# Kernel tuning notes

Measured on AMD Instinct MI355X. Metric: run time of the kernel, lower is better.

Reference implementation:

```python
import jax, jax.numpy as jnp
import numpy as np

H = 16            # num heads
D = 64            # head dim
HID = 1024        # hidden size
ALPHA = 1.0       # < 2 -> power-law kernel
BANDWIDTH = 1.0
A = 0.5           # doubly-stochastic exponent
RADIUS = 1.0      # sphere radius
EPS = 1e-7


def setup_inputs() -> dict:
    key = jax.random.key(0)
    ks = jax.random.split(key, 5)
    x = jax.random.normal(ks[0], (2, 2048, HID), dtype=jnp.float32)
    s = 1.0 / np.sqrt(HID)
    qkv_w = jax.random.normal(ks[1], (3 * HID, HID), dtype=jnp.float32) * s
    qkv_b = jnp.zeros((3 * HID,), dtype=jnp.float32)
    out_w = jax.random.normal(ks[2], (HID, HID), dtype=jnp.float32) * s
    out_b = jnp.zeros((HID,), dtype=jnp.float32)
    return {"x": x, "qkv_w": qkv_w, "qkv_b": qkv_b, "out_w": out_w, "out_b": out_b}


def _l2norm(t):
    # torch F.normalize(p=2, dim=-1): divide by max(||t||, 1e-12)
    n = jnp.sqrt(jnp.sum(t * t, axis=-1, keepdims=True))
    return t / jnp.maximum(n, 1e-12)


def reference(x, qkv_w, qkv_b, out_w, out_b):
    B, S, _ = x.shape
    qkv = x @ qkv_w.T + qkv_b                       # [B,S,3*HID]
    q, k, v = jnp.split(qkv, 3, axis=-1)
    # [B,H,S,D]
    q = _l2norm(q.reshape(B, S, H, D).transpose(0, 2, 1, 3))
    k = _l2norm(k.reshape(B, S, H, D).transpose(0, 2, 1, 3))
    v = v.reshape(B, S, H, D).transpose(0, 2, 1, 3)
    # geodesic distance on the sphere
    cos = jnp.clip(jnp.einsum('bhsd,bhtd->bhst', q, k), -1.0 + EPS, 1.0 - EPS)
    g_dist = jnp.arccos(cos) * RADIUS               # [B,H,S,S]
    # alpha < 2: power-law kernel
    attn_score = (1.0 + g_dist / jnp.sqrt(BANDWIDTH)) ** (-(D + ALPHA))
    # doubly-stochastic-style rescale: diag(row^-a) @ K @ diag(col^-a)
    row = attn_score.sum(-1) ** (-A)                # [B,H,S]
    col = attn_score.sum(-2) ** (-A)                # [B,H,S]
    k_tilde = row[..., :, None] * attn_score * col[..., None, :]
    # F.normalize(p=1, dim=3): divide by max(sum |.|, 1e-12); entries >= 0
    probs = k_tilde / jnp.maximum(k_tilde.sum(-1, keepdims=True), 1e-12)
    out = jnp.einsum('bhst,bhtd->bhsd', probs, v)   # [B,H,S,D]
    out = out.transpose(0, 2, 1, 3).reshape(B, S, HID)
    return out @ out_w.T + out_b
```

## Files before the change

kernel.cpp:

```cpp
#include <hip/hip_runtime.h>
#include <math.h>

#define NH   16
#define HD   64
#define HIDN 1024
#define NB   2
#define SEQ  2048
#define ROWS (NB*SEQ)
#define BH   (NB*NH)

typedef __attribute__((ext_vector_type(8))) short bf16x8;
typedef __attribute__((ext_vector_type(8))) _Float16 f16x8;
typedef __attribute__((ext_vector_type(4))) float f32x4;
typedef __attribute__((ext_vector_type(2))) float f32x2;
typedef _Float16 f16;

typedef const __attribute__((address_space(1))) void GV;
typedef __attribute__((address_space(3))) void LV;
__device__ __forceinline__ void glds16(const void* g, void* l) {
    __builtin_amdgcn_global_load_lds((GV*)g, (LV*)l, 16, 0, 0);
}

__device__ __forceinline__ unsigned short f2bf(float f) {
    unsigned u = __float_as_uint(f);
    u += 0x7FFF + ((u >> 16) & 1);
    return (unsigned short)(u >> 16);
}
__device__ __forceinline__ bf16x8 ldfrag(const unsigned short* p) {
    return *(const bf16x8*)p;
}
__device__ __forceinline__ f16x8 ldfragh(const f16* p) {
    return *(const f16x8*)p;
}
__device__ __forceinline__ f32x4 mfma16(bf16x8 a, bf16x8 b, f32x4 c) {
    return __builtin_amdgcn_mfma_f32_16x16x32_bf16(a, b, c, 0, 0, 0);
}
__device__ __forceinline__ f32x4 mfma16h(f16x8 a, f16x8 b, f32x4 c) {
    return __builtin_amdgcn_mfma_f32_16x16x32_f16(a, b, c, 0, 0, 0);
}

__device__ __forceinline__ f32x2 log2_1pacos_pair(float c0, float c1) {
    f32x2 u = { fmaxf(1.0f - c0, 0.0f), fmaxf(1.0f - c1, 0.0f) };
    f32x2 s = { __builtin_amdgcn_sqrtf(u.x), __builtin_amdgcn_sqrtf(u.y) };
    f32x2 p = u * 2.68532e-3f + 7.89259e-3f;
    p = u * p + 2.6516504e-2f;
    p = u * p + 1.1785113e-1f;
    p = u * p + 1.4142136f;
    f32x2 t = s * p + 1.0f;
    return (f32x2){ __builtin_amdgcn_logf(t.x), __builtin_amdgcn_logf(t.y) };
}
__device__ __forceinline__ unsigned packbf(f32x2 w) {
    return (__float_as_uint(w.x) >> 16) | (__float_as_uint(w.y) & 0xffff0000u);
}

__global__ __launch_bounds__(256)
void conv_f16(const float* __restrict__ src, f16* __restrict__ dst) {
    int i = (blockIdx.x * 256 + threadIdx.x) * 8;
    float4 a = *(const float4*)(src + i);
    float4 b = *(const float4*)(src + i + 4);
    f16x8 o = { (f16)a.x, (f16)a.y, (f16)a.z, (f16)a.w,
                (f16)b.x, (f16)b.y, (f16)b.z, (f16)b.w };
    *(f16x8*)(dst + i) = o;
}

__global__ __launch_bounds__(256)
void gemm_nt_f16(const f16* __restrict__ A, const f16* __restrict__ B,
                 const float* __restrict__ bias, float* __restrict__ C,
                 int M, int N, int K)
{
    __shared__ f16 As[128 * 32];
    __shared__ f16 Bs[128 * 32];
    const int tid = threadIdx.x;
    const int lane = tid & 63, w = tid >> 6;
    const int ln = lane & 15, lq = lane >> 4;
    const int wm = (w >> 1) * 64, wn = (w & 1) * 64;
    const int m0 = blockIdx.x * 128, n0 = blockIdx.y * 128;

    const int grow = lane >> 2;
    const int gcol = (lane & 3) * 8;
    const f16* Ab = A + (size_t)(m0 + w * 32 + grow) * K + gcol;
    const f16* Bb = B + (size_t)(n0 + w * 32 + grow) * K + gcol;
    f16* Asw = As + (w * 32) * 32;
    f16* Bsw = Bs + (w * 32) * 32;

    f32x4 acc[4][4];
    #pragma unroll
    for (int i = 0; i < 4; ++i)
        #pragma unroll
        for (int j = 0; j < 4; ++j) acc[i][j] = (f32x4){0.f, 0.f, 0.f, 0.f};

    for (int kc = 0; kc < K; kc += 32) {
        __syncthreads();
        #pragma unroll
        for (int i = 0; i < 2; ++i) {
            glds16(Ab + (size_t)(i * 16) * K + kc, Asw + (i * 16) * 32);
            glds16(Bb + (size_t)(i * 16) * K + kc, Bsw + (i * 16) * 32);
        }
        __syncthreads();
        f16x8 af[4], bf[4];
        #pragma unroll
        for (int i = 0; i < 4; ++i)
            af[i] = *(const f16x8*)&As[(wm + i * 16 + ln) * 32 + lq * 8];
        #pragma unroll
        for (int j = 0; j < 4; ++j)
            bf[j] = *(const f16x8*)&Bs[(wn + j * 16 + ln) * 32 + lq * 8];
        #pragma unroll
        for (int i = 0; i < 4; ++i)
            #pragma unroll
            for (int j = 0; j < 4; ++j)
                acc[i][j] = mfma16h(af[i], bf[j], acc[i][j]);
    }

    #pragma unroll
    for (int i = 0; i < 4; ++i) {
        #pragma unroll
        for (int j = 0; j < 4; ++j) {
            int colIdx = n0 + wn + j * 16 + ln;
            float bs = bias[colIdx];
            #pragma unroll
            for (int r = 0; r < 4; ++r) {
                int row = m0 + wm + i * 16 + lq * 4 + r;
                C[(size_t)row * N + colIdx] = acc[i][j][r] + bs;
            }
        }
    }
}

__global__ __launch_bounds__(256)
void normalize_qk_f16(const float* __restrict__ qkv,
                      f16* __restrict__ qf, f16* __restrict__ kf)
{
    int w    = blockIdx.x * 4 + (threadIdx.x >> 6);
    int lane = threadIdx.x & 63;
    int n = w >> 4, h = w & 15;
    int b = n >> 11, s = n & 2047;
    const float* base = qkv + (size_t)n * 3 * HIDN + h * HD;
    float q = base[lane], k = base[HIDN + lane];
    float qs = q * q, ks = k * k;
    #pragma unroll
    for (int o = 32; o; o >>= 1) { qs += __shfl_xor(qs, o); ks += __shfl_xor(ks, o); }
    q *= 1.0f / fmaxf(sqrtf(qs), 1e-12f);
    k *= 1.0f / fmaxf(sqrtf(ks), 1e-12f);
    size_t idx = ((size_t)((b * NH + h) * SEQ + s)) * HD + lane;
    qf[idx] = (f16)q;
    kf[idx] = (f16)k;
}

__global__ __launch_bounds__(256)
void v_transpose(const float* __restrict__ qkv, unsigned short* __restrict__ vth)
{
    __shared__ float Ls[64][65];
    int bh = blockIdx.y, s0 = blockIdx.x * 64;
    int b = bh >> 4, h = bh & 15;
    int tid = threadIdx.x;
    #pragma unroll
    for (int i = 0; i < 4; ++i) {
        int idx = tid + i * 256;
        int row = idx >> 4, c4 = (idx & 15) * 4;
        float4 v = *(const float4*)&qkv[((size_t)(b * SEQ + s0 + row)) * 3 * HIDN
                                        + 2 * HIDN + h * HD + c4];
        Ls[row][c4+0] = v.x; Ls[row][c4+1] = v.y; Ls[row][c4+2] = v.z; Ls[row][c4+3] = v.w;
    }
    __syncthreads();
    int d = tid >> 2, sb = (tid & 3) * 16;
    unsigned short hi[16];
    #pragma unroll
    for (int j = 0; j < 16; ++j) hi[j] = f2bf(Ls[sb + j][d]);
    size_t o = ((size_t)bh * HD + d) * SEQ + s0 + sb;
    *(uint4*)&vth[o]     = *(uint4*)&hi[0];
    *(uint4*)&vth[o + 8] = *(uint4*)&hi[8];
}

#define KSTR 72

__global__ __launch_bounds__(256)
void col_sum_f16(const f16* __restrict__ qf, const f16* __restrict__ kf,
                 float* __restrict__ colp)
{
    __shared__ __align__(16) f16 Qs[64 * KSTR];
    int bh = blockIdx.y;
    int tid = threadIdx.x, w = tid >> 6, lane = tid & 63, ln = lane & 15, lq = lane >> 4;
    int m0 = blockIdx.x * 64 + w * 16;
    const f16* qb = qf + (size_t)bh * SEQ * HD;
    const int sr = tid >> 3;
    const int sc = (tid & 7) * 8;

    size_t rowK = ((size_t)bh * SEQ + m0 + ln) * HD;
    f16x8 kf0 = ldfragh(kf + rowK + lq * 8), kf1 = ldfragh(kf + rowK + 32 + lq * 8);

    uint4 qa = *(const uint4*)(qb + (size_t)sr * HD + sc);
    uint4 qc = *(const uint4*)(qb + (size_t)(sr + 32) * HD + sc);

    f32x2 cacc01 = {0.f, 0.f}, cacc23 = {0.f, 0.f};
    #pragma unroll 1
    for (int st = 0; st < SEQ / 64; ++st) {
        __syncthreads();
        *(uint4*)&Qs[sr * KSTR + sc] = qa;
        *(uint4*)&Qs[(sr + 32) * KSTR + sc] = qc;
        int sn = (st + 1 < SEQ / 64) ? (st + 1) * 64 : 0;
        qa = *(const uint4*)(qb + (size_t)(sn + sr) * HD + sc);
        qc = *(const uint4*)(qb + (size_t)(sn + sr + 32) * HD + sc);
        __syncthreads();
        #pragma unroll
        for (int nt = 0; nt < 4; ++nt) {
            const f16* qp = &Qs[(nt * 16 + ln) * KSTR + lq * 8];
            f32x4 sacc = {0.f, 0.f, 0.f, 0.f};
            sacc = mfma16h(kf0, *(const f16x8*)qp, sacc);
            sacc = mfma16h(kf1, *(const f16x8*)(qp + 32), sacc);
            f32x2 l01 = log2_1pacos_pair(sacc[0], sacc[1]) * -65.0f;
            f32x2 l23 = log2_1pacos_pair(sacc[2], sacc[3]) * -65.0f;
            cacc01 += (f32x2){ __builtin_amdgcn_exp2f(l01.x),
                               __builtin_amdgcn_exp2f(l01.y) };
            cacc23 += (f32x2){ __builtin_amdgcn_exp2f(l23.x),
                               __builtin_amdgcn_exp2f(l23.y) };
        }
    }
    float cacc[4] = {cacc01.x, cacc01.y, cacc23.x, cacc23.y};
    #pragma unroll
    for (int r = 0; r < 4; ++r) {
        float v = cacc[r];
        v += __shfl_xor(v, 1); v += __shfl_xor(v, 2);
        v += __shfl_xor(v, 4); v += __shfl_xor(v, 8);
        if (ln == 0)
            colp[(size_t)bh * SEQ + m0 + lq * 4 + r] = v;
    }
}

__global__ __launch_bounds__(256)
void col_finalize(const float* __restrict__ colp, float* __restrict__ col)
{
    int i = (blockIdx.x * 256 + threadIdx.x) * 4;
    float4 a = *(const float4*)&colp[i];
    float4 o;
    o.x = -0.5f * __builtin_amdgcn_logf(a.x);
    o.y = -0.5f * __builtin_amdgcn_logf(a.y);
    o.z = -0.5f * __builtin_amdgcn_logf(a.z);
    o.w = -0.5f * __builtin_amdgcn_logf(a.w);
    *(float4*)&col[i] = o;
}

__global__ __launch_bounds__(256)
void attn_f16(const f16* __restrict__ qf, const f16* __restrict__ kf,
              const unsigned short* __restrict__ vth,
              const float* __restrict__ col, f16* __restrict__ ctx)
{
    __shared__ __align__(16) f16 Ks[64 * KSTR];
    __shared__ __align__(16) unsigned short Vs[64 * KSTR];
    __shared__ __align__(16) unsigned short Ws[4][16 * KSTR];
    __shared__ __align__(16) float lcls[64];
    int bh = blockIdx.y;
    int b = bh >> 4, h = bh & 15;
    int tid = threadIdx.x, w = tid >> 6, lane = tid & 63, ln = lane & 15, lq = lane >> 4;
    int m0 = blockIdx.x * 64 + w * 16;
    unsigned short* ws = Ws[w];

    const f16* kb = kf + (size_t)bh * SEQ * HD;
    const unsigned short* vb = vth + (size_t)bh * HD * SEQ;
    const float* cb = col + (size_t)bh * SEQ;

    const int sr = tid >> 3;
    const int sc = (tid & 7) * 8;

    size_t rowQ = ((size_t)bh * SEQ + m0 + ln) * HD;
    f16x8 qf0 = ldfragh(qf + rowQ + lq * 8), qf1 = ldfragh(qf + rowQ + 32 + lq * 8);

    bf16x8 ones;
    #pragma unroll
    for (int i = 0; i < 8; ++i) ones[i] = (short)0x3F80;

    f32x4 num[4];
    #pragma unroll
    for (int nt = 0; nt < 4; ++nt) num[nt] = (f32x4){0.f, 0.f, 0.f, 0.f};
    f32x4 den = {0.f, 0.f, 0.f, 0.f};

    uint4 ka = *(const uint4*)(kb + (size_t)sr * HD + sc);
    uint4 kc = *(const uint4*)(kb + (size_t)(sr + 32) * HD + sc);
    uint4 va = *(const uint4*)(vb + (size_t)sr * SEQ + sc);
    uint4 vc = *(const uint4*)(vb + (size_t)(sr + 32) * SEQ + sc);
    float clv = (tid < 64) ? cb[tid] : 0.f;

    #pragma unroll 1
    for (int tt = 0; tt < SEQ / 64; ++tt) {
        __syncthreads();
        *(uint4*)&Ks[sr * KSTR + sc] = ka;
        *(uint4*)&Ks[(sr + 32) * KSTR + sc] = kc;
        *(uint4*)&Vs[sr * KSTR + sc] = va;
        *(uint4*)&Vs[(sr + 32) * KSTR + sc] = vc;
        if (tid < 64) lcls[tid] = clv;
        int tn = (tt + 1 < SEQ / 64) ? (tt + 1) * 64 : 0;
        ka = *(const uint4*)(kb + (size_t)(tn + sr) * HD + sc);
        kc = *(const uint4*)(kb + (size_t)(tn + sr + 32) * HD + sc);
        va = *(const uint4*)(vb + (size_t)sr * SEQ + tn + sc);
        vc = *(const uint4*)(vb + (size_t)(sr + 32) * SEQ + tn + sc);
        clv = (tid < 64) ? cb[tn + tid] : 0.f;
        __syncthreads();

        #pragma unroll
        for (int nt = 0; nt < 4; ++nt) {
            const f16* kp = &Ks[(nt * 16 + ln) * KSTR + lq * 8];
            f32x4 sacc = {0.f, 0.f, 0.f, 0.f};
            sacc = mfma16h(*(const f16x8*)kp, qf0, sacc);
            sacc = mfma16h(*(const f16x8*)(kp + 32), qf1, sacc);
            float4 cl = *(const float4*)&lcls[nt * 16 + lq * 4];
            f32x2 a01 = log2_1pacos_pair(sacc[0], sacc[1]) * -65.0f
                        + (f32x2){cl.x, cl.y};
            f32x2 a23 = log2_1pacos_pair(sacc[2], sacc[3]) * -65.0f
                        + (f32x2){cl.z, cl.w};
            f32x2 w01 = { __builtin_amdgcn_exp2f(a01.x),
                          __builtin_amdgcn_exp2f(a01.y) };
            f32x2 w23 = { __builtin_amdgcn_exp2f(a23.x),
                          __builtin_amdgcn_exp2f(a23.y) };
            uint2 pw;
            pw.x = packbf(w01);
            pw.y = packbf(w23);
            *(uint2*)(ws + ln * KSTR + nt * 16 + lq * 4) = pw;
        }
        bf16x8 wa0 = ldfrag(ws + ln * KSTR + lq * 8);
        bf16x8 wa1 = ldfrag(ws + ln * KSTR + 32 + lq * 8);
        den = mfma16(wa0, ones, den);
        den = mfma16(wa1, ones, den);
        #pragma unroll
        for (int nt = 0; nt < 4; ++nt) {
            const unsigned short* vp = &Vs[(nt * 16 + ln) * KSTR + lq * 8];
            num[nt] = mfma16(wa0, *(const bf16x8*)vp, num[nt]);
            num[nt] = mfma16(wa1, *(const bf16x8*)(vp + 32), num[nt]);
        }
    }

    #pragma unroll
    for (int r = 0; r < 4; ++r) {
        float inv = 1.0f / fmaxf(den[r], 1e-12f);
        int s = m0 + lq * 4 + r;
        #pragma unroll
        for (int nt = 0; nt < 4; ++nt)
            ctx[((size_t)(b * SEQ + s)) * HIDN + h * HD + nt * 16 + ln] =
                (f16)(num[nt][r] * inv);
    }
}

extern "C" void kernel_launch(void* const* d_in, const int* in_sizes, int n_in,
                              void* d_out, int out_size, void* d_ws, size_t ws_size,
                              hipStream_t stream) {
    const float* x      = (const float*)d_in[0];
    const float* qkv_w  = (const float*)d_in[1];
    const float* qkv_b  = (const float*)d_in[2];
    const float* out_w  = (const float*)d_in[3];
    const float* out_b  = (const float*)d_in[4];
    float* out = (float*)d_out;

    const size_t NTT = (size_t)BH * SEQ * HD;
    float* qkv = (float*)d_ws;
    float* colp = qkv;
    float* col = qkv + (size_t)ROWS * 3 * HIDN;
    f16* xh    = (f16*)(col + (size_t)BH * SEQ);
    f16* wqh   = xh + (size_t)ROWS * HIDN;
    f16* woh   = wqh + (size_t)3 * HIDN * HIDN;
    f16* ctxh  = woh + (size_t)HIDN * HIDN;
    f16* qfp   = ctxh + (size_t)ROWS * HIDN;
    f16* kfp   = qfp + NTT;
    unsigned short* vth = (unsigned short*)(kfp + NTT);

    conv_f16<<<ROWS*HIDN/2048, 256, 0, stream>>>(x, xh);
    conv_f16<<<3*HIDN*HIDN/2048, 256, 0, stream>>>(qkv_w, wqh);
    conv_f16<<<HIDN*HIDN/2048, 256, 0, stream>>>(out_w, woh);

    gemm_nt_f16<<<dim3(ROWS/128, 3*HIDN/128), 256, 0, stream>>>(
        xh, wqh, qkv_b, qkv, ROWS, 3*HIDN, HIDN);
    normalize_qk_f16<<<ROWS*NH/4, 256, 0, stream>>>(qkv, qfp, kfp);
    v_transpose<<<dim3(SEQ/64, BH), 256, 0, stream>>>(qkv, vth);
    col_sum_f16<<<dim3(SEQ/64, BH), 256, 0, stream>>>(qfp, kfp, colp);
    col_finalize<<<BH*SEQ/1024, 256, 0, stream>>>(colp, col);
    attn_f16<<<dim3(SEQ/64, BH), 256, 0, stream>>>(qfp, kfp, vth, col, ctxh);
    gemm_nt_f16<<<dim3(ROWS/128, HIDN/128), 256, 0, stream>>>(
        ctxh, woh, out_b, out, ROWS, HIDN, HIDN);
}
```

Measured before the change: 327.1 us.

## Split key dimension in two for col-sum and attention kernels with reduction pass

Adds a grid z-dimension of 2 to col_sum and attn, so each block handles half of the key sequence. Partial column sums, numerators and denominators are written to workspace and combined in col_finalize and a new finalize_ctx kernel. This doubles the block count, from 1024 per kernel, to improve occupancy and tail balance on the GPU. The cost is extra fp32 partial-result traffic and one more kernel launch.

```diff
diff --git a/kernel.cpp b/kernel.cpp
--- a/kernel.cpp
+++ b/kernel.cpp
@@ -181,6 +181,7 @@
     int bh = blockIdx.y;
     int tid = threadIdx.x, w = tid >> 6, lane = tid & 63, ln = lane & 15, lq = lane >> 4;
     int m0 = blockIdx.x * 64 + w * 16;
+    const int sb0 = blockIdx.z * (SEQ / 128);
     const f16* qb = qf + (size_t)bh * SEQ * HD;
     const int sr = tid >> 3;
     const int sc = (tid & 7) * 8;
@@ -188,16 +189,16 @@
     size_t rowK = ((size_t)bh * SEQ + m0 + ln) * HD;
     f16x8 kf0 = ldfragh(kf + rowK + lq * 8), kf1 = ldfragh(kf + rowK + 32 + lq * 8);
 
-    uint4 qa = *(const uint4*)(qb + (size_t)sr * HD + sc);
-    uint4 qc = *(const uint4*)(qb + (size_t)(sr + 32) * HD + sc);
+    uint4 qa = *(const uint4*)(qb + (size_t)(sb0 * 64 + sr) * HD + sc);
+    uint4 qc = *(const uint4*)(qb + (size_t)(sb0 * 64 + sr + 32) * HD + sc);
 
     f32x2 cacc01 = {0.f, 0.f}, cacc23 = {0.f, 0.f};
     #pragma unroll 1
-    for (int st = 0; st < SEQ / 64; ++st) {
+    for (int st = sb0; st < sb0 + SEQ / 128; ++st) {
         __syncthreads();
         *(uint4*)&Qs[sr * KSTR + sc] = qa;
         *(uint4*)&Qs[(sr + 32) * KSTR + sc] = qc;
-        int sn = (st + 1 < SEQ / 64) ? (st + 1) * 64 : 0;
+        int sn = (st + 1 < sb0 + SEQ / 128) ? (st + 1) * 64 : sb0 * 64;
         qa = *(const uint4*)(qb + (size_t)(sn + sr) * HD + sc);
         qc = *(const uint4*)(qb + (size_t)(sn + sr + 32) * HD + sc);
         __syncthreads();
@@ -222,7 +223,7 @@
         v += __shfl_xor(v, 1); v += __shfl_xor(v, 2);
         v += __shfl_xor(v, 4); v += __shfl_xor(v, 8);
         if (ln == 0)
-            colp[(size_t)bh * SEQ + m0 + lq * 4 + r] = v;
+            colp[(size_t)blockIdx.z * BH * SEQ + (size_t)bh * SEQ + m0 + lq * 4 + r] = v;
     }
 }
 
@@ -231,18 +232,20 @@
 {
     int i = (blockIdx.x * 256 + threadIdx.x) * 4;
     float4 a = *(const float4*)&colp[i];
+    float4 b = *(const float4*)&colp[(size_t)BH * SEQ + i];
     float4 o;
-    o.x = -0.5f * __builtin_amdgcn_logf(a.x);
-    o.y = -0.5f * __builtin_amdgcn_logf(a.y);
-    o.z = -0.5f * __builtin_amdgcn_logf(a.z);
-    o.w = -0.5f * __builtin_amdgcn_logf(a.w);
+    o.x = -0.5f * __builtin_amdgcn_logf(a.x + b.x);
+    o.y = -0.5f * __builtin_amdgcn_logf(a.y + b.y);
+    o.z = -0.5f * __builtin_amdgcn_logf(a.z + b.z);
+    o.w = -0.5f * __builtin_amdgcn_logf(a.w + b.w);
     *(float4*)&col[i] = o;
 }
 
 __global__ __launch_bounds__(256)
 void attn_f16(const f16* __restrict__ qf, const f16* __restrict__ kf,
               const unsigned short* __restrict__ vth,
-              const float* __restrict__ col, f16* __restrict__ ctx)
+              const float* __restrict__ col,
+              float* __restrict__ numb, float* __restrict__ denb)
 {
     __shared__ __align__(16) f16 Ks[64 * KSTR];
     __shared__ __align__(16) unsigned short Vs[64 * KSTR];
@@ -252,6 +255,8 @@
     int b = bh >> 4, h = bh & 15;
     int tid = threadIdx.x, w = tid >> 6, lane = tid & 63, ln = lane & 15, lq = lane >> 4;
     int m0 = blockIdx.x * 64 + w * 16;
+    const int th = blockIdx.z;
+    const int tb = th * (SEQ / 128);
     unsigned short* ws = Ws[w];
 
     const f16* kb = kf + (size_t)bh * SEQ * HD;
@@ -273,21 +278,21 @@
     for (int nt = 0; nt < 4; ++nt) num[nt] = (f32x4){0.f, 0.f, 0.f, 0.f};
     f32x4 den = {0.f, 0.f, 0.f, 0.f};
 
-    uint4 ka = *(const uint4*)(kb + (size_t)sr * HD + sc);
-    uint4 kc = *(const uint4*)(kb + (size_t)(sr + 32) * HD + sc);
-    uint4 va = *(const uint4*)(vb + (size_t)sr * SEQ + sc);
-    uint4 vc = *(const uint4*)(vb + (size_t)(sr + 32) * SEQ + sc);
-    float clv = (tid < 64) ? cb[tid] : 0.f;
+    uint4 ka = *(const uint4*)(kb + (size_t)(tb * 64 + sr) * HD + sc);
+    uint4 kc = *(const uint4*)(kb + (size_t)(tb * 64 + sr + 32) * HD + sc);
+    uint4 va = *(const uint4*)(vb + (size_t)sr * SEQ + tb * 64 + sc);
+    uint4 vc = *(const uint4*)(vb + (size_t)(sr + 32) * SEQ + tb * 64 + sc);
+    float clv = (tid < 64) ? cb[tb * 64 + tid] : 0.f;
 
     #pragma unroll 1
-    for (int tt = 0; tt < SEQ / 64; ++tt) {
+    for (int tt = tb; tt < tb + SEQ / 128; ++tt) {
         __syncthreads();
         *(uint4*)&Ks[sr * KSTR + sc] = ka;
         *(uint4*)&Ks[(sr + 32) * KSTR + sc] = kc;
         *(uint4*)&Vs[sr * KSTR + sc] = va;
         *(uint4*)&Vs[(sr + 32) * KSTR + sc] = vc;
         if (tid < 64) lcls[tid] = clv;
-        int tn = (tt + 1 < SEQ / 64) ? (tt + 1) * 64 : 0;
+        int tn = (tt + 1 < tb + SEQ / 128) ? (tt + 1) * 64 : tb * 64;
         ka = *(const uint4*)(kb + (size_t)(tn + sr) * HD + sc);
         kc = *(const uint4*)(kb + (size_t)(tn + sr + 32) * HD + sc);
         va = *(const uint4*)(vb + (size_t)sr * SEQ + tn + sc);
@@ -327,15 +332,41 @@
         }
     }
 
+    const size_t noff = (size_t)th * ROWS * HIDN;
     #pragma unroll
     for (int r = 0; r < 4; ++r) {
-        float inv = 1.0f / fmaxf(den[r], 1e-12f);
         int s = m0 + lq * 4 + r;
         #pragma unroll
         for (int nt = 0; nt < 4; ++nt)
-            ctx[((size_t)(b * SEQ + s)) * HIDN + h * HD + nt * 16 + ln] =
-                (f16)(num[nt][r] * inv);
-    }
+            numb[noff + ((size_t)(b * SEQ + s)) * HIDN + h * HD + nt * 16 + ln] =
+                num[nt][r];
+        if (ln == 0)
+            denb[(size_t)th * BH * SEQ + (size_t)bh * SEQ + s] = den[r];
+    }
+}
+
+__global__ __launch_bounds__(256)
+void finalize_ctx(const float* __restrict__ numb, const float* __restrict__ denb,
+                  f16* __restrict__ ctx)
+{
+    size_t i = ((size_t)blockIdx.x * 256 + threadIdx.x) * 8;
+    int row = (int)(i >> 10);
+    int cidx = (int)(i & (HIDN - 1));
+    int b = row >> 11, s = row & 2047;
+    int h = cidx >> 6;
+    size_t di = (size_t)(b * NH + h) * SEQ + s;
+    float d = denb[di] + denb[(size_t)BH * SEQ + di];
+    float inv = 1.0f / fmaxf(d, 1e-12f);
+    const float* n1 = numb + (size_t)ROWS * HIDN;
+    float4 a0 = *(const float4*)&numb[i];
+    float4 a1 = *(const float4*)&numb[i + 4];
+    float4 b0 = *(const float4*)&n1[i];
+    float4 b1 = *(const float4*)&n1[i + 4];
+    f16x8 o = { (f16)((a0.x + b0.x) * inv), (f16)((a0.y + b0.y) * inv),
+                (f16)((a0.z + b0.z) * inv), (f16)((a0.w + b0.w) * inv),
+                (f16)((a1.x + b1.x) * inv), (f16)((a1.y + b1.y) * inv),
+                (f16)((a1.z + b1.z) * inv), (f16)((a1.w + b1.w) * inv) };
+    *(f16x8*)(ctx + i) = o;
 }
 
 extern "C" void kernel_launch(void* const* d_in, const int* in_sizes, int n_in,
@@ -351,6 +382,8 @@
     const size_t NTT = (size_t)BH * SEQ * HD;
     float* qkv = (float*)d_ws;
     float* colp = qkv;
+    float* denb = qkv + 2 * (size_t)BH * SEQ;
+    float* numb = qkv + 4 * (size_t)BH * SEQ;
     float* col = qkv + (size_t)ROWS * 3 * HIDN;
     f16* xh    = (f16*)(col + (size_t)BH * SEQ);
     f16* wqh   = xh + (size_t)ROWS * HIDN;
@@ -368,9 +401,11 @@
         xh, wqh, qkv_b, qkv, ROWS, 3*HIDN, HIDN);
     normalize_qk_f16<<<ROWS*NH/4, 256, 0, stream>>>(qkv, qfp, kfp);
     v_transpose<<<dim3(SEQ/64, BH), 256, 0, stream>>>(qkv, vth);
-    col_sum_f16<<<dim3(SEQ/64, BH), 256, 0, stream>>>(qfp, kfp, colp);
+    col_sum_f16<<<dim3(SEQ/64, BH, 2), 256, 0, stream>>>(qfp, kfp, colp);
     col_finalize<<<BH*SEQ/1024, 256, 0, stream>>>(colp, col);
-    attn_f16<<<dim3(SEQ/64, BH), 256, 0, stream>>>(qfp, kfp, vth, col, ctxh);
+    attn_f16<<<dim3(SEQ/64, BH, 2), 256, 0, stream>>>(qfp, kfp, vth, col,
+                                                      numb, denb);
+    finalize_ctx<<<ROWS*HIDN/2048, 256, 0, stream>>>(numb, denb, ctxh);
     gemm_nt_f16<<<dim3(ROWS/128, HIDN/128), 256, 0, stream>>>(
         ctxh, woh, out_b, out, ROWS, HIDN, HIDN);
 }
```

Result: faster. 317.8 us (-2.8%).
